# Optimization experiments

Measured on AMD Instinct MI355X. Metric: run time of the kernel, lower is better.

Reference implementation:

```python
import jax, jax.numpy as jnp
import numpy as np
from jax import lax

EPS = 1e-5
W_BITS = 8
A_BITS = 8


def _ste_round(x):
    # straight-through round (brevitas-style)
    return x + lax.stop_gradient(jnp.round(x) - x)


def weight_fake_quant(w, bits=W_BITS):
    # symmetric per-output-channel int quant: scale = max|w| / (2^(b-1)-1)
    qmax = float(2 ** (bits - 1) - 1)
    s = jnp.max(jnp.abs(w), axis=(1, 2, 3), keepdims=True) / qmax
    s = jnp.maximum(s, 1e-8)
    return jnp.clip(_ste_round(w / s), -qmax, qmax) * s


def quant_relu(x, scale, bits=A_BITS):
    # QuantReLU: relu then unsigned fake-quant with learned per-tensor scale
    qmax = float(2 ** bits - 1)
    s = jnp.maximum(scale, 1e-6)
    return jnp.clip(_ste_round(jax.nn.relu(x) / s), 0.0, qmax) * s


def conv2d(x, w, stride=1, padding=0):
    return lax.conv_general_dilated(
        x, w, window_strides=(stride, stride),
        padding=[(padding, padding), (padding, padding)],
        dimension_numbers=('NCHW', 'OIHW', 'NCHW'))


def batchnorm(x, gamma, beta, mean, var):
    # eval-mode BN with running stats
    inv = gamma / jnp.sqrt(var + EPS)
    return x * inv[None, :, None, None] + (beta - mean * inv)[None, :, None, None]


def setup_inputs() -> dict:
    key = jax.random.key(0)
    ks = jax.random.split(key, 20)
    B, Cin, P, H, W = 64, 1024, 256, 14, 14
    inp = {
        'x': jax.random.normal(ks[0], (B, Cin, H, W), jnp.float32),
        'w1': jax.random.normal(ks[1], (P, Cin, 1, 1), jnp.float32) * 0.05,
        'w2': jax.random.normal(ks[2], (P, P, 3, 3), jnp.float32) * 0.05,
        'w3': jax.random.normal(ks[3], (Cin, P, 1, 1), jnp.float32) * 0.05,
        'bn1_gamma': jax.random.uniform(ks[4], (P,), jnp.float32, 0.5, 1.5),
        'bn1_beta': jax.random.normal(ks[5], (P,), jnp.float32) * 0.1,
        'bn1_mean': jax.random.normal(ks[6], (P,), jnp.float32) * 0.1,
        'bn1_var': jax.random.uniform(ks[7], (P,), jnp.float32, 0.5, 1.5),
        'bn2_gamma': jax.random.uniform(ks[8], (P,), jnp.float32, 0.5, 1.5),
        'bn2_beta': jax.random.normal(ks[9], (P,), jnp.float32) * 0.1,
        'bn2_mean': jax.random.normal(ks[10], (P,), jnp.float32) * 0.1,
        'bn2_var': jax.random.uniform(ks[11], (P,), jnp.float32, 0.5, 1.5),
        'bn3_gamma': jax.random.uniform(ks[12], (Cin,), jnp.float32, 0.5, 1.5),
        'bn3_beta': jax.random.normal(ks[13], (Cin,), jnp.float32) * 0.1,
        'bn3_mean': jax.random.normal(ks[14], (Cin,), jnp.float32) * 0.1,
        'bn3_var': jax.random.uniform(ks[15], (Cin,), jnp.float32, 0.5, 1.5),
        's1': jax.random.uniform(ks[16], (1,), jnp.float32, 0.02, 0.1),
        's2': jax.random.uniform(ks[17], (1,), jnp.float32, 0.02, 0.1),
        's3': jax.random.uniform(ks[18], (1,), jnp.float32, 0.02, 0.1),
    }
    return inp


def reference(x, w1, w2, w3,
              bn1_gamma, bn1_beta, bn1_mean, bn1_var,
              bn2_gamma, bn2_beta, bn2_mean, bn2_var,
              bn3_gamma, bn3_beta, bn3_mean, bn3_var,
              s1, s2, s3):
    identity = x
    out = conv2d(x, weight_fake_quant(w1))
    out = batchnorm(out, bn1_gamma, bn1_beta, bn1_mean, bn1_var)
    out = quant_relu(out, s1)
    out = conv2d(out, weight_fake_quant(w2), stride=1, padding=1)
    out = batchnorm(out, bn2_gamma, bn2_beta, bn2_mean, bn2_var)
    out = quant_relu(out, s2)
    out = conv2d(out, weight_fake_quant(w3))
    out = batchnorm(out, bn3_gamma, bn3_beta, bn3_mean, bn3_var)
    out = out + identity  # downsample=None -> identity skip
    out = quant_relu(out, s3)
    return out
```

## Files before the change

### kernel.cpp

```cpp
#include <hip/hip_runtime.h>
#include <stdint.h>
#include <stddef.h>

typedef unsigned short u16;
typedef unsigned int   u32;
typedef signed char    s8;
typedef int   i32x4 __attribute__((ext_vector_type(4)));
typedef float f32x4 __attribute__((ext_vector_type(4)));
typedef s8    s8x4  __attribute__((ext_vector_type(4)));
typedef u32   u32x4 __attribute__((ext_vector_type(4)));

#define DEVFN static __device__ __forceinline__

#define GLL(g, l) __builtin_amdgcn_global_load_lds( \
    (__attribute__((address_space(1))) void*)(g),   \
    (__attribute__((address_space(3))) void*)(l), 16, 0, 0)

#define NREAL 12544
#define NPAD  16384
#define GUARD_ROWS 32
#define SXI 4096.0f

DEVFN float blockReduceMax(float m) {
    for (int off = 32; off; off >>= 1) m = fmaxf(m, __shfl_xor(m, off));
    __shared__ float s[4];
    int lane = threadIdx.x & 63, w = threadIdx.x >> 6;
    if (lane == 0) s[w] = m;
    __syncthreads();
    return fmaxf(fmaxf(s[0], s[1]), fmaxf(s[2], s[3]));
}
DEVFN float blockReduceSum(float v) {
    for (int off = 32; off; off >>= 1) v += __shfl_xor(v, off);
    __shared__ float s[4];
    int lane = threadIdx.x & 63, w = threadIdx.x >> 6;
    __syncthreads();
    if (lane == 0) s[w] = v;
    __syncthreads();
    return s[0] + s[1] + s[2] + s[3];
}

__global__ __launch_bounds__(256) void k_prep(
    const float* __restrict__ w1, const float* __restrict__ w2, const float* __restrict__ w3,
    const float* __restrict__ x,
    const float* __restrict__ g1, const float* __restrict__ b1, const float* __restrict__ m1, const float* __restrict__ v1,
    const float* __restrict__ g2, const float* __restrict__ b2, const float* __restrict__ m2, const float* __restrict__ v2,
    const float* __restrict__ g3, const float* __restrict__ b3, const float* __restrict__ m3, const float* __restrict__ v3,
    const float* __restrict__ s1p, const float* __restrict__ s2p,
    s8* __restrict__ w1q8, s8* __restrict__ w2t8, s8* __restrict__ w3q8,
    float* __restrict__ a1, float* __restrict__ c1,
    float* __restrict__ a2, float* __restrict__ c2,
    float* __restrict__ a3, float* __restrict__ c3,
    s8* __restrict__ xq, s8* __restrict__ act1g)
{
    __shared__ float tile[64*197];
    const int bid = blockIdx.x, t = threadIdx.x;

    if (bid < 256) {
        int p = bid;
        const float* wr = w1 + (size_t)p * 1024;
        float v[4], mx = 0.f;
        for (int i = 0; i < 4; ++i) { v[i] = wr[t + i*256]; mx = fmaxf(mx, fabsf(v[i])); }
        mx = blockReduceMax(mx);
        float s = fmaxf(mx / 127.0f, 1e-8f);
        float qs = 0.f;
        for (int i = 0; i < 4; ++i) {
            float q = fminf(fmaxf(rintf(v[i] / s), -127.f), 127.f);
            s8 qb = (s8)(int)q;
            w1q8[(size_t)p*2048 + t + i*256]        = qb;
            w1q8[(size_t)p*2048 + 1024 + t + i*256] = qb;
            qs += q;
        }
        qs = blockReduceSum(qs);
        if (t == 0) {
            float s1 = fmaxf(s1p[0], 1e-6f);
            float inv = g1[p] / sqrtf(v1[p] + 1e-5f);
            float a = s * (1.0f / SXI) * inv / s1;
            a1[p] = a;
            c1[p] = (b1[p] - m1[p] * inv) / s1 + 128.0f * qs * a;
        }
    } else if (bid < 512) {
        int p = bid - 256;
        const float* wr = w2 + (size_t)p * 2304;
        float v[9], mx = 0.f;
        for (int i = 0; i < 9; ++i) { v[i] = wr[t + i*256]; mx = fmaxf(mx, fabsf(v[i])); }
        mx = blockReduceMax(mx);
        float s = fmaxf(mx / 127.0f, 1e-8f);
        float qs = 0.f;
        for (int i = 0; i < 9; ++i) {
            int f = t + i*256;
            int ci = f / 9, r = f - ci*9;
            float q = fminf(fmaxf(rintf(v[i] / s), -127.f), 127.f);
            w2t8[(size_t)p*2304 + r*256 + ci] = (s8)(int)q;
            qs += q;
        }
        qs = blockReduceSum(qs);
        if (t == 0) {
            float s1 = fmaxf(s1p[0], 1e-6f), s2 = fmaxf(s2p[0], 1e-6f);
            float inv = g2[p] / sqrtf(v2[p] + 1e-5f);
            float a = s * s1 * inv / s2;
            a2[p] = a;
            c2[p] = (b2[p] - m2[p] * inv) / s2 + 128.0f * qs * a;
        }
    } else if (bid < 1536) {
        int co = bid - 512;
        float v = w3[(size_t)co*256 + t];
        float mx = blockReduceMax(fabsf(v));
        float s = fmaxf(mx / 127.0f, 1e-8f);
        float q = fminf(fmaxf(rintf(v / s), -127.f), 127.f);
        w3q8[(size_t)co*256 + t] = (s8)(int)q;
        float qs = blockReduceSum(q);
        if (t == 0) {
            float s2 = fmaxf(s2p[0], 1e-6f);
            float inv = g3[co] / sqrtf(v3[co] + 1e-5f);
            float a = s * s2 * inv;
            a3[co] = a;
            c3[co] = (b3[co] - m3[co] * inv) + 128.0f * qs * a;
        }
    } else if (bid < 2560) {
        int sb = bid - 1536;
        int b = sb >> 4, cg = sb & 15;
        const float* xb = x + ((size_t)b*1024 + cg*64) * 196;
        for (int i = t; i < 3136; i += 256) {
            f32x4 v = *(const f32x4*)&xb[i*4];
            int g = i*4;
#pragma unroll
            for (int j = 0; j < 4; ++j) {
                int gg = g + j;
                tile[gg + gg/196] = v[j];
            }
        }
        __syncthreads();
        for (int i = t; i < 3136; i += 256) {
            int pos = i >> 4, c4 = (i & 15) << 2;
            s8x4 hi, lo;
#pragma unroll
            for (int j = 0; j < 4; ++j) {
                float v = tile[(c4 + j)*197 + pos];
                int xf = (int)rintf(v * SXI);
                xf = xf > 32767 ? 32767 : (xf < -32767 ? -32767 : xf);
                int h = xf >> 8;
                int l = xf - (h << 8) - 128;
                hi[j] = (s8)h;
                lo[j] = (s8)l;
            }
            size_t n = (size_t)(b*196 + pos);
            *(s8x4*)&xq[n*2048 + cg*64 + c4]        = hi;
            *(s8x4*)&xq[n*2048 + 1024 + cg*64 + c4] = lo;
        }
    } else {
        const int total16 = (NPAD + 2*GUARD_ROWS) * 256 / 16;
        u32x4 val; val[0] = val[1] = val[2] = val[3] = 0x80808080u;
        u32x4* dst = (u32x4*)act1g;
        for (int i = (bid - 2560)*256 + t; i < total16; i += 260*256) dst[i] = val;
    }
}

template<int CONV>
__global__ __launch_bounds__(256) void k_gemm(
    const s8* __restrict__ A, const s8* __restrict__ Bact,
    s8* __restrict__ actout,
    const float* __restrict__ ca, const float* __restrict__ cc,
    const float* __restrict__ xin, const float* __restrict__ s3p,
    float* __restrict__ outp)
{
    constexpr int KSA = CONV==1 ? 2048 : 256;
    constexpr int KSB = CONV==1 ? 2048 : 256;
    constexpr int NKT = CONV==1 ? 16 : 2;

    __shared__ s8 lA[3][128*128];
    __shared__ s8 lB[3][64*128];

    const int t = threadIdx.x;
    const int lane = t & 63, wv = t >> 6;
    const int n0 = blockIdx.x * 64, m0 = blockIdx.y * 128;

    i32x4 acc[4][2], accB[4][2];
#pragma unroll
    for (int i = 0; i < 4; ++i)
#pragma unroll
        for (int j = 0; j < 2; ++j) { acc[i][j] = i32x4{0,0,0,0}; accB[i][j] = i32x4{0,0,0,0}; }

    const int srA = wv*32 + (lane >> 3);
    const int srB = wv*16 + (lane >> 3);
    const int ssel = (((lane & 7) ^ ((lane >> 3) & 7))) * 16;
    const int wr = wv >> 1, wc = wv & 1;
    const int fr = lane & 15, fg = lane >> 4;
    const int fsw = (fr & 7) << 4;

    auto stageK = [&](int kt, int buf) {
#pragma unroll
        for (int c = 0; c < 4; ++c) {
            const s8* g = A + (size_t)(m0 + srA + c*8) * KSA + kt*128 + ssel;
            GLL(g, &lA[buf][(wv*32 + c*8) * 128]);
        }
#pragma unroll
        for (int c = 0; c < 2; ++c) {
            const s8* g = Bact + (ptrdiff_t)(n0 + srB + c*8) * KSB + kt*128 + ssel;
            GLL(g, &lB[buf][(wv*16 + c*8) * 128]);
        }
    };

    auto computeK = [&](int buf, i32x4 (&ac)[4][2]) {
        const s8* bA = &lA[buf][0];
        const s8* bB = &lB[buf][0];
        __builtin_amdgcn_s_setprio(1);
#pragma unroll
        for (int kk = 0; kk < 2; ++kk) {
            i32x4 af[4], bf[2];
#pragma unroll
            for (int m = 0; m < 4; ++m) {
                int row = wr*64 + m*16 + fr;
                af[m] = *(const i32x4*)(bA + row*128 + ((kk*64 + fg*16) ^ fsw));
            }
#pragma unroll
            for (int n = 0; n < 2; ++n) {
                int row = wc*32 + n*16 + fr;
                bf[n] = *(const i32x4*)(bB + row*128 + ((kk*64 + fg*16) ^ fsw));
            }
#pragma unroll
            for (int m = 0; m < 4; ++m)
#pragma unroll
                for (int n = 0; n < 2; ++n)
                    ac[m][n] = __builtin_amdgcn_mfma_i32_16x16x64_i8(af[m], bf[n], ac[m][n], 0, 0, 0);
        }
        __builtin_amdgcn_s_setprio(0);
    };

    stageK(0, 0);
    stageK(1, 1);
    asm volatile("s_waitcnt vmcnt(6)" ::: "memory");
    __builtin_amdgcn_s_barrier();

#pragma unroll
    for (int kt = 0; kt < NKT; ++kt) {
        const int buf = kt % 3;
        if (kt + 2 < NKT) stageK(kt + 2, (kt + 2) % 3);
        if (CONV == 1 && kt >= 8) computeK(buf, accB);
        else                      computeK(buf, acc);
        if (kt + 1 < NKT) {
            if (kt + 2 < NKT) { asm volatile("s_waitcnt vmcnt(6)" ::: "memory"); }
            else              { asm volatile("s_waitcnt vmcnt(0)" ::: "memory"); }
            __builtin_amdgcn_s_barrier();
        }
    }

    const int pb = m0 + wr*64 + fg*4;
    const int nb = n0 + wc*32 + fr;

    if constexpr (CONV == 1) {
        (void)xin; (void)s3p; (void)outp;
#pragma unroll
        for (int m = 0; m < 4; ++m) {
            int p0 = pb + m*16;
            float av[4], cv[4];
#pragma unroll
            for (int j = 0; j < 4; ++j) { av[j] = ca[p0+j]; cv[j] = cc[p0+j]; }
#pragma unroll
            for (int n = 0; n < 2; ++n) {
                int nn = nb + n*16;
                int b  = nn / 196;
                int pos = nn - b*196;
                int h = pos / 14, w = pos - h*14;
                int np = b*256 + (h+1)*16 + (w+1);
                s8x4 st;
#pragma unroll
                for (int j = 0; j < 4; ++j) {
                    float fa = 256.0f * (float)acc[m][n][j] + (float)accB[m][n][j];
                    float y = fmaxf(fa * av[j] + cv[j], 0.f);
                    int q = (int)fminf(rintf(y), 255.f);
                    st[j] = (s8)(q - 128);
                }
                *(s8x4*)&actout[(size_t)np*256 + p0] = st;
            }
        }
    } else {
        (void)actout;
        float s3 = fmaxf(s3p[0], 1e-6f);
        float rs3 = 1.0f / s3;
#pragma unroll
        for (int n = 0; n < 2; ++n) {
            int co = nb + n*16;
            float av = ca[co], cv = cc[co];
#pragma unroll
            for (int m = 0; m < 4; ++m) {
                int p4 = pb + m*16;
                int b  = p4 / 196;
                int hw = p4 - b*196;
                size_t off = ((size_t)((b << 10) + co))*196 + hw;
                f32x4 xv = *(const f32x4*)&xin[off];
                f32x4 st;
#pragma unroll
                for (int j = 0; j < 4; ++j) {
                    float y = fmaxf((float)acc[m][n][j] * av + cv + xv[j], 0.f);
                    float q = fminf(rintf(y * rs3), 255.f);
                    st[j] = q * s3;
                }
                *(f32x4*)&outp[off] = st;
            }
        }
    }
}

__global__ __launch_bounds__(512) void k_gemm2(
    const s8* __restrict__ A, const s8* __restrict__ Bact,
    s8* __restrict__ actout,
    const float* __restrict__ ca, const float* __restrict__ cc)
{
    constexpr int NKT = 18;

    __shared__ s8 lA[3][128*128];
    __shared__ s8 lB[3][128*128];

    const int t = threadIdx.x;
    const int lane = t & 63, wv = t >> 6;
    const int n0 = blockIdx.x * 128, m0 = blockIdx.y * 128;

    i32x4 acc[4][2];
#pragma unroll
    for (int i = 0; i < 4; ++i)
#pragma unroll
        for (int j = 0; j < 2; ++j) acc[i][j] = i32x4{0,0,0,0};

    const int srAB = wv*16 + (lane >> 3);
    const int ssel = (((lane & 7) ^ ((lane >> 3) & 7))) * 16;
    const int wr = wv >> 2, wc = wv & 3;
    const int fr = lane & 15, fg = lane >> 4;
    const int fsw = (fr & 7) << 4;

    auto stageK = [&](int kt, int buf) {
        int bcol = (kt & 1) * 128;
        int kpos = kt >> 1;
        int ky = kpos / 3, kx = kpos - ky*3;
        int bshift = (ky - 1)*16 + (kx - 1);
#pragma unroll
        for (int c = 0; c < 2; ++c) {
            const s8* g = A + (size_t)(m0 + srAB + c*8) * 2304 + kt*128 + ssel;
            GLL(g, &lA[buf][(wv*16 + c*8) * 128]);
        }
#pragma unroll
        for (int c = 0; c < 2; ++c) {
            const s8* g = Bact + (ptrdiff_t)(n0 + srAB + c*8 + bshift) * 256 + bcol + ssel;
            GLL(g, &lB[buf][(wv*16 + c*8) * 128]);
        }
    };

    auto computeK = [&](int buf) {
        const s8* bA = &lA[buf][0];
        const s8* bB = &lB[buf][0];
        __builtin_amdgcn_s_setprio(1);
#pragma unroll
        for (int kk = 0; kk < 2; ++kk) {
            i32x4 af[4], bf[2];
#pragma unroll
            for (int m = 0; m < 4; ++m) {
                int row = wr*64 + m*16 + fr;
                af[m] = *(const i32x4*)(bA + row*128 + ((kk*64 + fg*16) ^ fsw));
            }
#pragma unroll
            for (int n = 0; n < 2; ++n) {
                int row = wc*32 + n*16 + fr;
                bf[n] = *(const i32x4*)(bB + row*128 + ((kk*64 + fg*16) ^ fsw));
            }
#pragma unroll
            for (int m = 0; m < 4; ++m)
#pragma unroll
                for (int n = 0; n < 2; ++n)
                    acc[m][n] = __builtin_amdgcn_mfma_i32_16x16x64_i8(af[m], bf[n], acc[m][n], 0, 0, 0);
        }
        __builtin_amdgcn_s_setprio(0);
    };

    stageK(0, 0);
    stageK(1, 1);
    asm volatile("s_waitcnt vmcnt(4)" ::: "memory");
    __builtin_amdgcn_s_barrier();

#pragma unroll
    for (int kt = 0; kt < NKT; ++kt) {
        const int buf = kt % 3;
        if (kt + 2 < NKT) stageK(kt + 2, (kt + 2) % 3);
        computeK(buf);
        if (kt + 1 < NKT) {
            if (kt + 2 < NKT) { asm volatile("s_waitcnt vmcnt(4)" ::: "memory"); }
            else              { asm volatile("s_waitcnt vmcnt(0)" ::: "memory"); }
            __builtin_amdgcn_s_barrier();
        }
    }

    const int pb = m0 + wr*64 + fg*4;
    const int nb = n0 + wc*32 + fr;
#pragma unroll
    for (int m = 0; m < 4; ++m) {
        int p0 = pb + m*16;
        float av[4], cv[4];
#pragma unroll
        for (int j = 0; j < 4; ++j) { av[j] = ca[p0+j]; cv[j] = cc[p0+j]; }
#pragma unroll
        for (int n = 0; n < 2; ++n) {
            int nn = nb + n*16;
            int hp = (nn >> 4) & 15, wp = nn & 15;
            if (hp < 1 || hp > 14 || wp < 1 || wp > 14) continue;
            int np = (nn >> 8)*196 + (hp-1)*14 + (wp-1);
            s8x4 st;
#pragma unroll
            for (int j = 0; j < 4; ++j) {
                float y = fmaxf((float)acc[m][n][j] * av[j] + cv[j], 0.f);
                int q = (int)fminf(rintf(y), 255.f);
                st[j] = (s8)(q - 128);
            }
            *(s8x4*)&actout[(size_t)np*256 + p0] = st;
        }
    }
}

extern "C" void kernel_launch(void* const* d_in, const int* in_sizes, int n_in,
                              void* d_out, int out_size, void* d_ws, size_t ws_size,
                              hipStream_t stream) {
    (void)in_sizes; (void)n_in; (void)out_size; (void)ws_size;
    const float* x   = (const float*)d_in[0];
    const float* w1  = (const float*)d_in[1];
    const float* w2  = (const float*)d_in[2];
    const float* w3  = (const float*)d_in[3];
    const float* g1  = (const float*)d_in[4];
    const float* b1  = (const float*)d_in[5];
    const float* m1  = (const float*)d_in[6];
    const float* v1  = (const float*)d_in[7];
    const float* g2  = (const float*)d_in[8];
    const float* b2  = (const float*)d_in[9];
    const float* m2  = (const float*)d_in[10];
    const float* v2  = (const float*)d_in[11];
    const float* g3  = (const float*)d_in[12];
    const float* b3  = (const float*)d_in[13];
    const float* m3  = (const float*)d_in[14];
    const float* v3  = (const float*)d_in[15];
    const float* s1p = (const float*)d_in[16];
    const float* s2p = (const float*)d_in[17];
    const float* s3p = (const float*)d_in[18];
    float* out = (float*)d_out;

    char* w = (char*)d_ws;
    s8* w1q8 = (s8*)w;  w += (size_t)256*2048;
    s8* w2t8 = (s8*)w;  w += (size_t)256*2304;
    s8* w3q8 = (s8*)w;  w += (size_t)1024*256;
    float* a1 = (float*)w; w += 256*4;
    float* c1 = (float*)w; w += 256*4;
    float* a2 = (float*)w; w += 256*4;
    float* c2 = (float*)w; w += 256*4;
    float* a3 = (float*)w; w += 1024*4;
    float* c3 = (float*)w; w += 1024*4;
    s8* xq    = (s8*)w; w += (size_t)NREAL*2048;
    s8* act1g = (s8*)w; w += (size_t)(NPAD + 2*GUARD_ROWS)*256;
    s8* act1  = act1g + (size_t)GUARD_ROWS*256;
    s8* act2  = (s8*)w; w += (size_t)NREAL*256;

    k_prep<<<2820, 256, 0, stream>>>(w1, w2, w3, x,
                                     g1,b1,m1,v1, g2,b2,m2,v2, g3,b3,m3,v3,
                                     s1p, s2p,
                                     w1q8, w2t8, w3q8,
                                     a1,c1, a2,c2, a3,c3,
                                     xq, act1g);

    k_gemm<1><<<dim3(196, 2), 256, 0, stream>>>(w1q8, xq, act1, a1, c1, nullptr, nullptr, nullptr);
    k_gemm2<<<dim3(128, 2), 512, 0, stream>>>(w2t8, act1, act2, a2, c2);
    k_gemm<3><<<dim3(16, 98), 256, 0, stream>>>(act2, w3q8, nullptr, a3, c3, x, s3p, out);
}
```

Measured before the change: 204.9 us.

## Double K-tile depth to 256 in all three int8 GEMMs with reworked staging

Each GEMM now stages K tiles 256 bytes wide instead of 128, halving the number of K iterations and barriers. gemm1 keeps a triple buffer, which grows LDS to 144KB per block. gemm2 moves to a double buffer with a full vmcnt(0) wait each step, giving 128KB. gemm3 becomes a dedicated single-shot kernel with no pipeline. The swizzle for the global-to-LDS loads is redone for 256-byte rows. The trade-off is fewer barriers and less loop overhead against much larger LDS, which lowers occupancy to one block per CU and weakens load/compute overlap in gemm2.

```diff
diff --git a/kernel.cpp b/kernel.cpp
--- a/kernel.cpp
+++ b/kernel.cpp
@@ -155,20 +155,15 @@
     }
 }
 
-template<int CONV>
-__global__ __launch_bounds__(256) void k_gemm(
+
+__global__ __launch_bounds__(256) void k_gemm1(
     const s8* __restrict__ A, const s8* __restrict__ Bact,
     s8* __restrict__ actout,
-    const float* __restrict__ ca, const float* __restrict__ cc,
-    const float* __restrict__ xin, const float* __restrict__ s3p,
-    float* __restrict__ outp)
+    const float* __restrict__ ca, const float* __restrict__ cc)
 {
-    constexpr int KSA = CONV==1 ? 2048 : 256;
-    constexpr int KSB = CONV==1 ? 2048 : 256;
-    constexpr int NKT = CONV==1 ? 16 : 2;
-
-    __shared__ s8 lA[3][128*128];
-    __shared__ s8 lB[3][64*128];
+    constexpr int NKT = 8;
+    __shared__ s8 lA[3][128*256];
+    __shared__ s8 lB[3][64*256];
 
     const int t = threadIdx.x;
     const int lane = t & 63, wv = t >> 6;
@@ -180,23 +175,23 @@
 #pragma unroll
         for (int j = 0; j < 2; ++j) { acc[i][j] = i32x4{0,0,0,0}; accB[i][j] = i32x4{0,0,0,0}; }
 
-    const int srA = wv*32 + (lane >> 3);
-    const int srB = wv*16 + (lane >> 3);
-    const int ssel = (((lane & 7) ^ ((lane >> 3) & 7))) * 16;
+    const int rl = lane >> 4, cl = lane & 15;
+    const int sE = ((cl ^ rl) << 4);
+    const int sO = sE ^ 64;
     const int wr = wv >> 1, wc = wv & 1;
-    const int fr = lane & 15, fg = lane >> 4;
+    const int fr = cl, fg = rl;
     const int fsw = (fr & 7) << 4;
 
     auto stageK = [&](int kt, int buf) {
 #pragma unroll
+        for (int c = 0; c < 8; ++c) {
+            const s8* g = A + (size_t)(m0 + wv*32 + c*4 + rl) * 2048 + kt*256 + ((c & 1) ? sO : sE);
+            GLL(g, &lA[buf][(wv*32 + c*4) * 256]);
+        }
+#pragma unroll
         for (int c = 0; c < 4; ++c) {
-            const s8* g = A + (size_t)(m0 + srA + c*8) * KSA + kt*128 + ssel;
-            GLL(g, &lA[buf][(wv*32 + c*8) * 128]);
-        }
-#pragma unroll
-        for (int c = 0; c < 2; ++c) {
-            const s8* g = Bact + (ptrdiff_t)(n0 + srB + c*8) * KSB + kt*128 + ssel;
-            GLL(g, &lB[buf][(wv*16 + c*8) * 128]);
+            const s8* g = Bact + (size_t)(n0 + wv*16 + c*4 + rl) * 2048 + kt*256 + ((c & 1) ? sO : sE);
+            GLL(g, &lB[buf][(wv*16 + c*4) * 256]);
         }
     };
 
@@ -205,17 +200,17 @@
         const s8* bB = &lB[buf][0];
         __builtin_amdgcn_s_setprio(1);
 #pragma unroll
-        for (int kk = 0; kk < 2; ++kk) {
+        for (int kk = 0; kk < 4; ++kk) {
             i32x4 af[4], bf[2];
 #pragma unroll
             for (int m = 0; m < 4; ++m) {
                 int row = wr*64 + m*16 + fr;
-                af[m] = *(const i32x4*)(bA + row*128 + ((kk*64 + fg*16) ^ fsw));
+                af[m] = *(const i32x4*)(bA + row*256 + ((kk*64 + fg*16) ^ fsw));
             }
 #pragma unroll
             for (int n = 0; n < 2; ++n) {
                 int row = wc*32 + n*16 + fr;
-                bf[n] = *(const i32x4*)(bB + row*128 + ((kk*64 + fg*16) ^ fsw));
+                bf[n] = *(const i32x4*)(bB + row*256 + ((kk*64 + fg*16) ^ fsw));
             }
 #pragma unroll
             for (int m = 0; m < 4; ++m)
@@ -228,75 +223,46 @@
 
     stageK(0, 0);
     stageK(1, 1);
-    asm volatile("s_waitcnt vmcnt(6)" ::: "memory");
+    asm volatile("s_waitcnt vmcnt(12)" ::: "memory");
     __builtin_amdgcn_s_barrier();
 
 #pragma unroll
     for (int kt = 0; kt < NKT; ++kt) {
         const int buf = kt % 3;
         if (kt + 2 < NKT) stageK(kt + 2, (kt + 2) % 3);
-        if (CONV == 1 && kt >= 8) computeK(buf, accB);
-        else                      computeK(buf, acc);
+        if (kt >= 4) computeK(buf, accB);
+        else         computeK(buf, acc);
         if (kt + 1 < NKT) {
-            if (kt + 2 < NKT) { asm volatile("s_waitcnt vmcnt(6)" ::: "memory"); }
-            else              { asm volatile("s_waitcnt vmcnt(0)" ::: "memory"); }
+            if (kt + 2 < NKT) { asm volatile("s_waitcnt vmcnt(12)" ::: "memory"); }
+            else              { asm volatile("s_waitcnt vmcnt(0)"  ::: "memory"); }
             __builtin_amdgcn_s_barrier();
         }
     }
 
     const int pb = m0 + wr*64 + fg*4;
     const int nb = n0 + wc*32 + fr;
-
-    if constexpr (CONV == 1) {
-        (void)xin; (void)s3p; (void)outp;
-#pragma unroll
-        for (int m = 0; m < 4; ++m) {
-            int p0 = pb + m*16;
-            float av[4], cv[4];
-#pragma unroll
-            for (int j = 0; j < 4; ++j) { av[j] = ca[p0+j]; cv[j] = cc[p0+j]; }
-#pragma unroll
-            for (int n = 0; n < 2; ++n) {
-                int nn = nb + n*16;
-                int b  = nn / 196;
-                int pos = nn - b*196;
-                int h = pos / 14, w = pos - h*14;
-                int np = b*256 + (h+1)*16 + (w+1);
-                s8x4 st;
-#pragma unroll
-                for (int j = 0; j < 4; ++j) {
-                    float fa = 256.0f * (float)acc[m][n][j] + (float)accB[m][n][j];
-                    float y = fmaxf(fa * av[j] + cv[j], 0.f);
-                    int q = (int)fminf(rintf(y), 255.f);
-                    st[j] = (s8)(q - 128);
-                }
-                *(s8x4*)&actout[(size_t)np*256 + p0] = st;
-            }
-        }
-    } else {
-        (void)actout;
-        float s3 = fmaxf(s3p[0], 1e-6f);
-        float rs3 = 1.0f / s3;
+#pragma unroll
+    for (int m = 0; m < 4; ++m) {
+        int p0 = pb + m*16;
+        float av[4], cv[4];
+#pragma unroll
+        for (int j = 0; j < 4; ++j) { av[j] = ca[p0+j]; cv[j] = cc[p0+j]; }
 #pragma unroll
         for (int n = 0; n < 2; ++n) {
-            int co = nb + n*16;
-            float av = ca[co], cv = cc[co];
-#pragma unroll
-            for (int m = 0; m < 4; ++m) {
-                int p4 = pb + m*16;
-                int b  = p4 / 196;
-                int hw = p4 - b*196;
-                size_t off = ((size_t)((b << 10) + co))*196 + hw;
-                f32x4 xv = *(const f32x4*)&xin[off];
-                f32x4 st;
-#pragma unroll
-                for (int j = 0; j < 4; ++j) {
-                    float y = fmaxf((float)acc[m][n][j] * av + cv + xv[j], 0.f);
-                    float q = fminf(rintf(y * rs3), 255.f);
-                    st[j] = q * s3;
-                }
-                *(f32x4*)&outp[off] = st;
-            }
+            int nn = nb + n*16;
+            int b  = nn / 196;
+            int pos = nn - b*196;
+            int h = pos / 14, w = pos - h*14;
+            int np = b*256 + (h+1)*16 + (w+1);
+            s8x4 st;
+#pragma unroll
+            for (int j = 0; j < 4; ++j) {
+                float fa = 256.0f * (float)acc[m][n][j] + (float)accB[m][n][j];
+                float y = fmaxf(fa * av[j] + cv[j], 0.f);
+                int q = (int)fminf(rintf(y), 255.f);
+                st[j] = (s8)(q - 128);
+            }
+            *(s8x4*)&actout[(size_t)np*256 + p0] = st;
         }
     }
 }
@@ -306,10 +272,9 @@
     s8* __restrict__ actout,
     const float* __restrict__ ca, const float* __restrict__ cc)
 {
-    constexpr int NKT = 18;
-
-    __shared__ s8 lA[3][128*128];
-    __shared__ s8 lB[3][128*128];
+    constexpr int NKT = 9;
+    __shared__ s8 lA[2][128*256];
+    __shared__ s8 lB[2][128*256];
 
     const int t = threadIdx.x;
     const int lane = t & 63, wv = t >> 6;
@@ -321,26 +286,25 @@
 #pragma unroll
         for (int j = 0; j < 2; ++j) acc[i][j] = i32x4{0,0,0,0};
 
-    const int srAB = wv*16 + (lane >> 3);
-    const int ssel = (((lane & 7) ^ ((lane >> 3) & 7))) * 16;
+    const int rl = lane >> 4, cl = lane & 15;
+    const int sE = ((cl ^ rl) << 4);
+    const int sO = sE ^ 64;
     const int wr = wv >> 2, wc = wv & 3;
-    const int fr = lane & 15, fg = lane >> 4;
+    const int fr = cl, fg = rl;
     const int fsw = (fr & 7) << 4;
 
     auto stageK = [&](int kt, int buf) {
-        int bcol = (kt & 1) * 128;
-        int kpos = kt >> 1;
-        int ky = kpos / 3, kx = kpos - ky*3;
+        int ky = kt / 3, kx = kt - ky*3;
         int bshift = (ky - 1)*16 + (kx - 1);
 #pragma unroll
-        for (int c = 0; c < 2; ++c) {
-            const s8* g = A + (size_t)(m0 + srAB + c*8) * 2304 + kt*128 + ssel;
-            GLL(g, &lA[buf][(wv*16 + c*8) * 128]);
-        }
-#pragma unroll
-        for (int c = 0; c < 2; ++c) {
-            const s8* g = Bact + (ptrdiff_t)(n0 + srAB + c*8 + bshift) * 256 + bcol + ssel;
-            GLL(g, &lB[buf][(wv*16 + c*8) * 128]);
+        for (int c = 0; c < 4; ++c) {
+            const s8* g = A + (size_t)(m0 + wv*16 + c*4 + rl) * 2304 + kt*256 + ((c & 1) ? sO : sE);
+            GLL(g, &lA[buf][(wv*16 + c*4) * 256]);
+        }
+#pragma unroll
+        for (int c = 0; c < 4; ++c) {
+            const s8* g = Bact + (ptrdiff_t)(n0 + wv*16 + c*4 + rl + bshift) * 256 + ((c & 1) ? sO : sE);
+            GLL(g, &lB[buf][(wv*16 + c*4) * 256]);
         }
     };
 
@@ -349,17 +313,17 @@
         const s8* bB = &lB[buf][0];
         __builtin_amdgcn_s_setprio(1);
 #pragma unroll
-        for (int kk = 0; kk < 2; ++kk) {
+        for (int kk = 0; kk < 4; ++kk) {
             i32x4 af[4], bf[2];
 #pragma unroll
             for (int m = 0; m < 4; ++m) {
                 int row = wr*64 + m*16 + fr;
-                af[m] = *(const i32x4*)(bA + row*128 + ((kk*64 + fg*16) ^ fsw));
+                af[m] = *(const i32x4*)(bA + row*256 + ((kk*64 + fg*16) ^ fsw));
             }
 #pragma unroll
             for (int n = 0; n < 2; ++n) {
                 int row = wc*32 + n*16 + fr;
-                bf[n] = *(const i32x4*)(bB + row*128 + ((kk*64 + fg*16) ^ fsw));
+                bf[n] = *(const i32x4*)(bB + row*256 + ((kk*64 + fg*16) ^ fsw));
             }
 #pragma unroll
             for (int m = 0; m < 4; ++m)
@@ -371,19 +335,18 @@
     };
 
     stageK(0, 0);
-    stageK(1, 1);
-    asm volatile("s_waitcnt vmcnt(4)" ::: "memory");
+    asm volatile("s_waitcnt vmcnt(0)" ::: "memory");
     __builtin_amdgcn_s_barrier();
 
+    int b = 0;
 #pragma unroll
     for (int kt = 0; kt < NKT; ++kt) {
-        const int buf = kt % 3;
-        if (kt + 2 < NKT) stageK(kt + 2, (kt + 2) % 3);
-        computeK(buf);
+        if (kt + 1 < NKT) stageK(kt + 1, b ^ 1);
+        computeK(b);
         if (kt + 1 < NKT) {
-            if (kt + 2 < NKT) { asm volatile("s_waitcnt vmcnt(4)" ::: "memory"); }
-            else              { asm volatile("s_waitcnt vmcnt(0)" ::: "memory"); }
+            asm volatile("s_waitcnt vmcnt(0)" ::: "memory");
             __builtin_amdgcn_s_barrier();
+            b ^= 1;
         }
     }
 
@@ -409,6 +372,94 @@
                 st[j] = (s8)(q - 128);
             }
             *(s8x4*)&actout[(size_t)np*256 + p0] = st;
+        }
+    }
+}
+
+__global__ __launch_bounds__(256) void k_gemm3(
+    const s8* __restrict__ A, const s8* __restrict__ Bact,
+    const float* __restrict__ ca, const float* __restrict__ cc,
+    const float* __restrict__ xin, const float* __restrict__ s3p,
+    float* __restrict__ outp)
+{
+    __shared__ s8 lA[128*256];
+    __shared__ s8 lB[64*256];
+
+    const int t = threadIdx.x;
+    const int lane = t & 63, wv = t >> 6;
+    const int n0 = blockIdx.x * 64, m0 = blockIdx.y * 128;
+
+    i32x4 acc[4][2];
+#pragma unroll
+    for (int i = 0; i < 4; ++i)
+#pragma unroll
+        for (int j = 0; j < 2; ++j) acc[i][j] = i32x4{0,0,0,0};
+
+    const int rl = lane >> 4, cl = lane & 15;
+    const int sE = ((cl ^ rl) << 4);
+    const int sO = sE ^ 64;
+    const int wr = wv >> 1, wc = wv & 1;
+    const int fr = cl, fg = rl;
+    const int fsw = (fr & 7) << 4;
+
+#pragma unroll
+    for (int c = 0; c < 8; ++c) {
+        const s8* g = A + (size_t)(m0 + wv*32 + c*4 + rl) * 256 + ((c & 1) ? sO : sE);
+        GLL(g, &lA[(wv*32 + c*4) * 256]);
+    }
+#pragma unroll
+    for (int c = 0; c < 4; ++c) {
+        const s8* g = Bact + (size_t)(n0 + wv*16 + c*4 + rl) * 256 + ((c & 1) ? sO : sE);
+        GLL(g, &lB[(wv*16 + c*4) * 256]);
+    }
+    asm volatile("s_waitcnt vmcnt(0)" ::: "memory");
+    __builtin_amdgcn_s_barrier();
+
+    __builtin_amdgcn_s_setprio(1);
+#pragma unroll
+    for (int kk = 0; kk < 4; ++kk) {
+        i32x4 af[4], bf[2];
+#pragma unroll
+        for (int m = 0; m < 4; ++m) {
+            int row = wr*64 + m*16 + fr;
+            af[m] = *(const i32x4*)(&lA[0] + row*256 + ((kk*64 + fg*16) ^ fsw));
+        }
+#pragma unroll
+        for (int n = 0; n < 2; ++n) {
+            int row = wc*32 + n*16 + fr;
+            bf[n] = *(const i32x4*)(&lB[0] + row*256 + ((kk*64 + fg*16) ^ fsw));
+        }
+#pragma unroll
+        for (int m = 0; m < 4; ++m)
+#pragma unroll
+            for (int n = 0; n < 2; ++n)
+                acc[m][n] = __builtin_amdgcn_mfma_i32_16x16x64_i8(af[m], bf[n], acc[m][n], 0, 0, 0);
+    }
+    __builtin_amdgcn_s_setprio(0);
+
+    float s3 = fmaxf(s3p[0], 1e-6f);
+    float rs3 = 1.0f / s3;
+    const int pb = m0 + wr*64 + fg*4;
+    const int nb = n0 + wc*32 + fr;
+#pragma unroll
+    for (int n = 0; n < 2; ++n) {
+        int co = nb + n*16;
+        float av = ca[co], cv = cc[co];
+#pragma unroll
+        for (int m = 0; m < 4; ++m) {
+            int p4 = pb + m*16;
+            int b  = p4 / 196;
+            int hw = p4 - b*196;
+            size_t off = ((size_t)((b << 10) + co))*196 + hw;
+            f32x4 xv = *(const f32x4*)&xin[off];
+            f32x4 st;
+#pragma unroll
+            for (int j = 0; j < 4; ++j) {
+                float y = fmaxf((float)acc[m][n][j] * av + cv + xv[j], 0.f);
+                float q = fminf(rintf(y * rs3), 255.f);
+                st[j] = q * s3;
+            }
+            *(f32x4*)&outp[off] = st;
         }
     }
 }
@@ -460,7 +511,7 @@
                                      a1,c1, a2,c2, a3,c3,
                                      xq, act1g);
 
-    k_gemm<1><<<dim3(196, 2), 256, 0, stream>>>(w1q8, xq, act1, a1, c1, nullptr, nullptr, nullptr);
+    k_gemm1<<<dim3(196, 2), 256, 0, stream>>>(w1q8, xq, act1, a1, c1);
     k_gemm2<<<dim3(128, 2), 512, 0, stream>>>(w2t8, act1, act2, a2, c2);
-    k_gemm<3><<<dim3(16, 98), 256, 0, stream>>>(act2, w3q8, nullptr, a3, c3, x, s3p, out);
-}
+    k_gemm3<<<dim3(16, 98), 256, 0, stream>>>(act2, w3q8, a3, c3, x, s3p, out);
+}
```

New measurement: 210.8 us. 2.9% more time.
